# Kernel tuning notes

Hardware: AMD Instinct MI355X
Metric: run time of the kernel (lower is better)

## Reference

```python
import jax, jax.numpy as jnp
import numpy as np

N0, N1, N2 = 409600, 40960, 4096   # source / mid / target node counts per sampled layer
E1, E2 = 409600, 40960             # edges in layer 1 / layer 2
F_IN, F_HID, F_OUT = 512, 256, 128


def setup_inputs() -> dict:
    key = jax.random.key(0)
    ks = jax.random.split(key, 12)
    s = 1.0 / np.sqrt(F_IN)
    s2 = 1.0 / np.sqrt(F_HID)
    return {
        "x": jax.random.normal(ks[0], (N0, F_IN), dtype=jnp.float32),
        "ei1_src": jax.random.randint(ks[1], (E1,), 0, N0),
        "ei1_dst": jax.random.randint(ks[2], (E1,), 0, N1),
        "ei2_src": jax.random.randint(ks[3], (E2,), 0, N1),
        "ei2_dst": jax.random.randint(ks[4], (E2,), 0, N2),
        "W1l": jax.random.uniform(ks[5], (F_IN, F_HID), jnp.float32, -s, s),
        "b1": jax.random.uniform(ks[6], (F_HID,), jnp.float32, -s, s),
        "W1r": jax.random.uniform(ks[7], (F_IN, F_HID), jnp.float32, -s, s),
        "W2l": jax.random.uniform(ks[8], (F_HID, F_OUT), jnp.float32, -s2, s2),
        "b2": jax.random.uniform(ks[9], (F_OUT,), jnp.float32, -s2, s2),
        "W2r": jax.random.uniform(ks[10], (F_HID, F_OUT), jnp.float32, -s2, s2),
    }


def _sage(x_src, src, dst, n_dst, Wl, b, Wr):
    # PyG SAGEConv (mean aggr): out = lin_l(mean_j x_j) + lin_r(x_target)
    msg = x_src[src]                                           # [E, F] gather
    agg = jax.ops.segment_sum(msg, dst, num_segments=n_dst)    # [n_dst, F]
    cnt = jax.ops.segment_sum(jnp.ones((src.shape[0],), x_src.dtype), dst,
                              num_segments=n_dst)
    mean = agg / jnp.maximum(cnt, 1.0)[:, None]
    x_dst = x_src[:n_dst]                                      # targets are first
    return mean @ Wl + b + x_dst @ Wr


def reference(x, ei1_src, ei1_dst, ei2_src, ei2_dst, W1l, b1, W1r, W2l, b2, W2r):
    h = _sage(x, ei1_src, ei1_dst, N1, W1l, b1, W1r)           # [N1, F_HID]
    h = jax.nn.relu(h)                                         # dropout = identity (eval)
    out = _sage(h, ei2_src, ei2_dst, N2, W2l, b2, W2r)         # [N2, F_OUT]
    return out
```

## Files before the change

### kernel.cpp

```cpp
#include <hip/hip_runtime.h>
#include <hip/hip_bf16.h>

#define N0 409600
#define N1 40960
#define N2 4096
#define E1c 409600
#define E2c 40960
#define F_IN 512
#define F_HID 256
#define F_OUT 128

using bf16x8 = __attribute__((ext_vector_type(8))) short;
using f32x4  = __attribute__((ext_vector_type(4))) float;

__device__ __forceinline__ ushort f2bf(float f) {
    union { float f; unsigned u; } v; v.f = f;
    unsigned r = v.u + 0x7fffu + ((v.u >> 16) & 1u);
    return (ushort)(r >> 16);
}
__device__ __forceinline__ float bf2f(ushort b) {
    union { unsigned u; float f; } v; v.u = ((unsigned)b) << 16;
    return v.f;
}

__device__ __forceinline__ bf16x8 load8(const ushort* p) {
    return *(const bf16x8*)p;
}
__device__ __forceinline__ bf16x8 load8(const float* p) {
    float4 a = *(const float4*)p;
    float4 b = *(const float4*)(p + 4);
    bf16x8 r;
    r[0] = (short)f2bf(a.x); r[1] = (short)f2bf(a.y);
    r[2] = (short)f2bf(a.z); r[3] = (short)f2bf(a.w);
    r[4] = (short)f2bf(b.x); r[5] = (short)f2bf(b.y);
    r[6] = (short)f2bf(b.z); r[7] = (short)f2bf(b.w);
    return r;
}

__global__ void k_prep(const int* __restrict__ dst1, int* __restrict__ cnt1,
                       const int* __restrict__ dst2, int* __restrict__ cnt2,
                       const float* __restrict__ W1l, const float* __restrict__ W1r,
                       const float* __restrict__ W2l, const float* __restrict__ W2r,
                       ushort* __restrict__ W1lT, ushort* __restrict__ W1rT,
                       ushort* __restrict__ W2lT, ushort* __restrict__ W2rT) {
    int idx = blockIdx.x * blockDim.x + threadIdx.x;
    if (idx < E1c) atomicAdd(&cnt1[dst1[idx]], 1);
    else if (idx - E1c < E2c) atomicAdd(&cnt2[dst2[idx - E1c]], 1);
    const int S1 = F_IN * F_HID;
    const int S2 = F_HID * F_OUT;
    if (idx < S1) {
        int k = idx / F_HID, n = idx % F_HID;
        W1lT[(size_t)n * F_IN + k] = f2bf(W1l[idx]);
    } else if (idx < 2 * S1) {
        int j = idx - S1;
        int k = j / F_HID, n = j % F_HID;
        W1rT[(size_t)n * F_IN + k] = f2bf(W1r[j]);
    } else if (idx < 2 * S1 + S2) {
        int j = idx - 2 * S1;
        int k = j / F_OUT, n = j % F_OUT;
        W2lT[(size_t)n * F_HID + k] = f2bf(W2l[j]);
    } else if (idx < 2 * S1 + 2 * S2) {
        int j = idx - 2 * S1 - S2;
        int k = j / F_OUT, n = j % F_OUT;
        W2rT[(size_t)n * F_HID + k] = f2bf(W2r[j]);
    }
}

#define NBLK1 (N1 / 1024)
#define NBLK2 (N2 / 1024)

__global__ __launch_bounds__(1024) void k_scanA2(const int* __restrict__ cnt1, int* __restrict__ off1,
                                                 int* __restrict__ bsum1,
                                                 const int* __restrict__ cnt2, int* __restrict__ off2,
                                                 int* __restrict__ bsum2) {
    __shared__ int wsum[16];
    int blk = blockIdx.x;
    const int* cnt; int* off; int* bsum; int lb;
    if (blk < NBLK1) { cnt = cnt1; off = off1; bsum = bsum1; lb = blk; }
    else             { cnt = cnt2; off = off2; bsum = bsum2; lb = blk - NBLK1; }
    int t = threadIdx.x, lane = t & 63, w = t >> 6;
    int i = lb * 1024 + t;
    int v = cnt[i];
    int s = v;
#pragma unroll
    for (int d = 1; d < 64; d <<= 1) {
        int u = __shfl_up(s, d, 64);
        if (lane >= d) s += u;
    }
    if (lane == 63) wsum[w] = s;
    __syncthreads();
    int wpre = 0, total = 0;
#pragma unroll
    for (int j = 0; j < 16; j++) {
        int u = wsum[j];
        if (j < w) wpre += u;
        total += u;
    }
    off[i] = wpre + (s - v);
    if (t == 0) bsum[lb] = total;
}

__global__ __launch_bounds__(1024) void k_scanB2(int* __restrict__ off1, int* __restrict__ cur1,
                                                 const int* __restrict__ bsum1,
                                                 int* __restrict__ off2, int* __restrict__ cur2,
                                                 const int* __restrict__ bsum2) {
    __shared__ int s_pre, s_tot;
    int blk = blockIdx.x;
    int* off; int* cur; const int* bsum; int lb, nblk, n;
    if (blk < NBLK1) { off = off1; cur = cur1; bsum = bsum1; lb = blk;         nblk = NBLK1; n = N1; }
    else             { off = off2; cur = cur2; bsum = bsum2; lb = blk - NBLK1; nblk = NBLK2; n = N2; }
    int t = threadIdx.x;
    if (t < 64) {
        int v = (t < nblk) ? bsum[t] : 0;
        int p = (t < lb) ? v : 0;
        int tt = v;
#pragma unroll
        for (int d = 32; d >= 1; d >>= 1) {
            p  += __shfl_xor(p, d, 64);
            tt += __shfl_xor(tt, d, 64);
        }
        if (t == 0) { s_pre = p; s_tot = tt; }
    }
    __syncthreads();
    int i = lb * 1024 + t;
    int val = off[i] + s_pre;
    off[i] = val;
    cur[i] = val;
    if (lb == 0 && t == 0) off[n] = s_tot;
}

__global__ void k_scatter2(const int* __restrict__ src1, const int* __restrict__ dst1,
                           int* __restrict__ cur1, int* __restrict__ perm1,
                           const int* __restrict__ src2, const int* __restrict__ dst2,
                           int* __restrict__ cur2, int* __restrict__ perm2) {
    int e = blockIdx.x * blockDim.x + threadIdx.x;
    if (e < E1c) {
        int d = dst1[e];
        int pos = atomicAdd(&cur1[d], 1);
        perm1[pos] = src1[e];
    } else {
        int e2 = e - E1c;
        if (e2 < E2c) {
            int d = dst2[e2];
            int pos = atomicAdd(&cur2[d], 1);
            perm2[pos] = src2[e2];
        }
    }
}

__global__ void k_agg1(const float* __restrict__ x, const int* __restrict__ perm,
                       const int* __restrict__ off, ushort* __restrict__ mean) {
    int d = blockIdx.x;
    int beg = off[d], end = off[d + 1];
    int t = threadIdx.x;
    const float4* xp = (const float4*)x;
    float ax = 0.f, ay = 0.f, az = 0.f, aw = 0.f;
    int e = beg;
    for (; e + 3 < end; e += 4) {
        int s0 = perm[e], s1 = perm[e + 1], s2 = perm[e + 2], s3 = perm[e + 3];
        float4 v0 = xp[(size_t)s0 * (F_IN / 4) + t];
        float4 v1 = xp[(size_t)s1 * (F_IN / 4) + t];
        float4 v2 = xp[(size_t)s2 * (F_IN / 4) + t];
        float4 v3 = xp[(size_t)s3 * (F_IN / 4) + t];
        ax += (v0.x + v1.x) + (v2.x + v3.x);
        ay += (v0.y + v1.y) + (v2.y + v3.y);
        az += (v0.z + v1.z) + (v2.z + v3.z);
        aw += (v0.w + v1.w) + (v2.w + v3.w);
    }
    for (; e < end; e++) {
        float4 v0 = xp[(size_t)perm[e] * (F_IN / 4) + t];
        ax += v0.x; ay += v0.y; az += v0.z; aw += v0.w;
    }
    int deg = end - beg;
    float inv = 1.0f / (float)(deg > 0 ? deg : 1);
    ushort4 o;
    o.x = f2bf(ax * inv); o.y = f2bf(ay * inv);
    o.z = f2bf(az * inv); o.w = f2bf(aw * inv);
    ((ushort4*)mean)[(size_t)d * (F_IN / 4) + t] = o;
}

__global__ void k_agg2(const ushort* __restrict__ h, const int* __restrict__ perm,
                       const int* __restrict__ off, ushort* __restrict__ mean) {
    int d = blockIdx.x;
    int beg = off[d], end = off[d + 1];
    int t = threadIdx.x;
    const ushort4* hp = (const ushort4*)h;
    float a0 = 0.f, a1 = 0.f, a2 = 0.f, a3 = 0.f;
    int e = beg;
    for (; e + 3 < end; e += 4) {
        ushort4 v = hp[(size_t)perm[e] * (F_HID / 4) + t];
        ushort4 u = hp[(size_t)perm[e + 1] * (F_HID / 4) + t];
        ushort4 w = hp[(size_t)perm[e + 2] * (F_HID / 4) + t];
        ushort4 z = hp[(size_t)perm[e + 3] * (F_HID / 4) + t];
        a0 += (bf2f(v.x) + bf2f(u.x)) + (bf2f(w.x) + bf2f(z.x));
        a1 += (bf2f(v.y) + bf2f(u.y)) + (bf2f(w.y) + bf2f(z.y));
        a2 += (bf2f(v.z) + bf2f(u.z)) + (bf2f(w.z) + bf2f(z.z));
        a3 += (bf2f(v.w) + bf2f(u.w)) + (bf2f(w.w) + bf2f(z.w));
    }
    for (; e < end; e++) {
        ushort4 v = hp[(size_t)perm[e] * (F_HID / 4) + t];
        a0 += bf2f(v.x); a1 += bf2f(v.y); a2 += bf2f(v.z); a3 += bf2f(v.w);
    }
    int deg = end - beg;
    float inv = 1.0f / (float)(deg > 0 ? deg : 1);
    ushort4 o;
    o.x = f2bf(a0 * inv); o.y = f2bf(a1 * inv);
    o.z = f2bf(a2 * inv); o.w = f2bf(a3 * inv);
    ((ushort4*)mean)[(size_t)d * (F_HID / 4) + t] = o;
}

#define GBK 32
#define APAD 8
template<int WM, int WN, int MF, int NF, int K, int MINW, typename TA2>
__global__ __launch_bounds__(256, MINW) void k_gemm(
    const ushort* __restrict__ A1, const TA2* __restrict__ A2,
    const ushort* __restrict__ B1T, const ushort* __restrict__ B2T,
    const float* __restrict__ bias, int M, int N, int relu,
    ushort* __restrict__ Cb, float* __restrict__ Cf)
{
    constexpr int BM = WM * MF * 16;
    constexpr int BN = WN * NF * 16;
    constexpr int KS = K / GBK;
    constexpr int NS = 2 * KS;
    static_assert(BM % 64 == 0 && BN % 64 == 0, "tile must be multiple of 64");
    __shared__ ushort As[2][BM][GBK + APAD];
    __shared__ ushort Bs[2][BN][GBK + APAD];
    int tid = threadIdx.x;
    int lane = tid & 63;
    int wid = tid >> 6;
    int wm = wid / WN, wn = wid % WN;
    int bm = blockIdx.x * BM, bn = blockIdx.y * BN;

    f32x4 acc[MF][NF];
#pragma unroll
    for (int i = 0; i < MF; i++)
#pragma unroll
        for (int j = 0; j < NF; j++) acc[i][j] = (f32x4){0.f, 0.f, 0.f, 0.f};

    int sr = tid >> 2;
    int sc = (tid & 3) * 8;
    int r0 = lane & 15, kq = (lane >> 4) * 8;

    bf16x8 ra[BM / 64], rb[BN / 64];
#pragma unroll
    for (int i = 0; i < BM / 64; i++)
        ra[i] = load8(A1 + (size_t)(bm + sr + i * 64) * K + sc);
#pragma unroll
    for (int i = 0; i < BN / 64; i++)
        rb[i] = load8(B1T + (size_t)(bn + sr + i * 64) * K + sc);

    for (int s = 0; s < NS; ++s) {
        int buf = s & 1;
#pragma unroll
        for (int i = 0; i < BM / 64; i++) *(bf16x8*)&As[buf][sr + i * 64][sc] = ra[i];
#pragma unroll
        for (int i = 0; i < BN / 64; i++) *(bf16x8*)&Bs[buf][sr + i * 64][sc] = rb[i];
        __syncthreads();
        if (s + 1 < NS) {
            int s1 = s + 1;
            int part1 = (s1 >= KS) ? 1 : 0;
            int k01 = (s1 - part1 * KS) * GBK;
#pragma unroll
            for (int i = 0; i < BM / 64; i++) {
                size_t idx = (size_t)(bm + sr + i * 64) * K + k01 + sc;
                ra[i] = part1 ? load8(A2 + idx) : load8(A1 + idx);
            }
            const ushort* __restrict__ B = part1 ? B2T : B1T;
#pragma unroll
            for (int i = 0; i < BN / 64; i++)
                rb[i] = load8(B + (size_t)(bn + sr + i * 64) * K + k01 + sc);
        }
        bf16x8 af[MF], bfr[NF];
#pragma unroll
        for (int i = 0; i < MF; i++)
            af[i] = *(const bf16x8*)&As[buf][wm * (MF * 16) + i * 16 + r0][kq];
#pragma unroll
        for (int j = 0; j < NF; j++)
            bfr[j] = *(const bf16x8*)&Bs[buf][wn * (NF * 16) + j * 16 + r0][kq];
#pragma unroll
        for (int i = 0; i < MF; i++)
#pragma unroll
            for (int j = 0; j < NF; j++)
                acc[i][j] = __builtin_amdgcn_mfma_f32_16x16x32_bf16(af[i], bfr[j], acc[i][j], 0, 0, 0);
    }

    int cn0 = lane & 15;
    int rq = (lane >> 4) * 4;
#pragma unroll
    for (int i = 0; i < MF; i++) {
#pragma unroll
        for (int j = 0; j < NF; j++) {
            int col = bn + wn * (NF * 16) + j * 16 + cn0;
            float bv = bias[col];
#pragma unroll
            for (int rr = 0; rr < 4; rr++) {
                int row = bm + wm * (MF * 16) + i * 16 + rq + rr;
                float v = acc[i][j][rr] + bv;
                if (relu) v = fmaxf(v, 0.f);
                if (Cb) Cb[(size_t)row * N + col] = f2bf(v);
                if (Cf) Cf[(size_t)row * N + col] = v;
            }
        }
    }
}

static inline size_t align256(size_t x) { return (x + 255) & ~(size_t)255; }

extern "C" void kernel_launch(void* const* d_in, const int* in_sizes, int n_in,
                              void* d_out, int out_size, void* d_ws, size_t ws_size,
                              hipStream_t stream) {
    const float* x = (const float*)d_in[0];
    const int* ei1_src = (const int*)d_in[1];
    const int* ei1_dst = (const int*)d_in[2];
    const int* ei2_src = (const int*)d_in[3];
    const int* ei2_dst = (const int*)d_in[4];
    const float* W1l = (const float*)d_in[5];
    const float* b1 = (const float*)d_in[6];
    const float* W1r = (const float*)d_in[7];
    const float* W2l = (const float*)d_in[8];
    const float* b2 = (const float*)d_in[9];
    const float* W2r = (const float*)d_in[10];
    float* out = (float*)d_out;

    char* p = (char*)d_ws;
    size_t o = 0;
    int* cnt1 = (int*)(p + o); o += (size_t)N1 * 4;
    int* cnt2 = (int*)(p + o); o = align256(o + (size_t)N2 * 4);
    int* off1 = (int*)(p + o); o = align256(o + (size_t)(N1 + 1) * 4);
    int* cur1 = (int*)(p + o); o = align256(o + (size_t)N1 * 4);
    int* perm1 = (int*)(p + o); o = align256(o + (size_t)E1c * 4);
    int* off2 = (int*)(p + o); o = align256(o + (size_t)(N2 + 1) * 4);
    int* cur2 = (int*)(p + o); o = align256(o + (size_t)N2 * 4);
    int* perm2 = (int*)(p + o); o = align256(o + (size_t)E2c * 4);
    int* bsum1 = (int*)(p + o); o = align256(o + 64 * 4);
    int* bsum2 = (int*)(p + o); o = align256(o + 64 * 4);
    ushort* mean1 = (ushort*)(p + o); o = align256(o + (size_t)N1 * F_IN * 2);
    ushort* h     = (ushort*)(p + o); o = align256(o + (size_t)N1 * F_HID * 2);
    ushort* mean2 = (ushort*)(p + o); o = align256(o + (size_t)N2 * F_HID * 2);
    ushort* W1lT  = (ushort*)(p + o); o = align256(o + (size_t)F_IN * F_HID * 2);
    ushort* W1rT  = (ushort*)(p + o); o = align256(o + (size_t)F_IN * F_HID * 2);
    ushort* W2lT  = (ushort*)(p + o); o = align256(o + (size_t)F_HID * F_OUT * 2);
    ushort* W2rT  = (ushort*)(p + o); o = align256(o + (size_t)F_HID * F_OUT * 2);

    hipMemsetAsync(cnt1, 0, (size_t)(N1 + N2) * 4, stream);

    {
        int total = E1c + E2c;
        k_prep<<<(total + 255) / 256, 256, 0, stream>>>(
            ei1_dst, cnt1, ei2_dst, cnt2,
            W1l, W1r, W2l, W2r, W1lT, W1rT, W2lT, W2rT);
    }
    k_scanA2<<<NBLK1 + NBLK2, 1024, 0, stream>>>(cnt1, off1, bsum1, cnt2, off2, bsum2);
    k_scanB2<<<NBLK1 + NBLK2, 1024, 0, stream>>>(off1, cur1, bsum1, off2, cur2, bsum2);
    k_scatter2<<<(E1c + E2c + 255) / 256, 256, 0, stream>>>(
        ei1_src, ei1_dst, cur1, perm1, ei2_src, ei2_dst, cur2, perm2);

    k_agg1<<<N1, F_IN / 4, 0, stream>>>(x, perm1, off1, mean1);
    {
        dim3 grid(N1 / 64, F_HID / 256);
        k_gemm<1, 4, 4, 4, F_IN, 3, float><<<grid, 256, 0, stream>>>(
            mean1, x, W1lT, W1rT, b1, N1, F_HID, 1, h, nullptr);
    }

    k_agg2<<<N2, F_HID / 4, 0, stream>>>(h, perm2, off2, mean2);
    {
        dim3 grid(N2 / 64, F_OUT / 64);
        k_gemm<2, 2, 2, 2, F_HID, 4, ushort><<<grid, 256, 0, stream>>>(
            mean2, h, W2lT, W2rT, b2, N2, F_OUT, 0, nullptr, out);
    }
}
```

Measured before the change: 264.6 us.

## Load GEMM B fragments directly from global to registers and unroll agg1 gather by 8

The GEMM no longer stages the weight (B) tile in shared memory. Each wave loads its MFMA B fragments straight from global memory into registers and double-buffers them across k-steps, which removes the LDS writes and reads for B and frees shared memory. The trade-off is that B data is no longer shared between waves, so global and L2 traffic for weights goes up along with register pressure. The layer-1 aggregation loop is also unrolled to 8 outstanding gathers to expose more memory-level parallelism.

Measured after the change: 278.9 us. 1.05x slower.

```diff
diff --git a/kernel.cpp b/kernel.cpp
--- a/kernel.cpp
+++ b/kernel.cpp
@@ -156,12 +156,25 @@
     const float4* xp = (const float4*)x;
     float ax = 0.f, ay = 0.f, az = 0.f, aw = 0.f;
     int e = beg;
+    for (; e + 7 < end; e += 8) {
+        float4 v0 = xp[(size_t)perm[e]     * (F_IN / 4) + t];
+        float4 v1 = xp[(size_t)perm[e + 1] * (F_IN / 4) + t];
+        float4 v2 = xp[(size_t)perm[e + 2] * (F_IN / 4) + t];
+        float4 v3 = xp[(size_t)perm[e + 3] * (F_IN / 4) + t];
+        float4 v4 = xp[(size_t)perm[e + 4] * (F_IN / 4) + t];
+        float4 v5 = xp[(size_t)perm[e + 5] * (F_IN / 4) + t];
+        float4 v6 = xp[(size_t)perm[e + 6] * (F_IN / 4) + t];
+        float4 v7 = xp[(size_t)perm[e + 7] * (F_IN / 4) + t];
+        ax += ((v0.x + v1.x) + (v2.x + v3.x)) + ((v4.x + v5.x) + (v6.x + v7.x));
+        ay += ((v0.y + v1.y) + (v2.y + v3.y)) + ((v4.y + v5.y) + (v6.y + v7.y));
+        az += ((v0.z + v1.z) + (v2.z + v3.z)) + ((v4.z + v5.z) + (v6.z + v7.z));
+        aw += ((v0.w + v1.w) + (v2.w + v3.w)) + ((v4.w + v5.w) + (v6.w + v7.w));
+    }
     for (; e + 3 < end; e += 4) {
-        int s0 = perm[e], s1 = perm[e + 1], s2 = perm[e + 2], s3 = perm[e + 3];
-        float4 v0 = xp[(size_t)s0 * (F_IN / 4) + t];
-        float4 v1 = xp[(size_t)s1 * (F_IN / 4) + t];
-        float4 v2 = xp[(size_t)s2 * (F_IN / 4) + t];
-        float4 v3 = xp[(size_t)s3 * (F_IN / 4) + t];
+        float4 v0 = xp[(size_t)perm[e]     * (F_IN / 4) + t];
+        float4 v1 = xp[(size_t)perm[e + 1] * (F_IN / 4) + t];
+        float4 v2 = xp[(size_t)perm[e + 2] * (F_IN / 4) + t];
+        float4 v3 = xp[(size_t)perm[e + 3] * (F_IN / 4) + t];
         ax += (v0.x + v1.x) + (v2.x + v3.x);
         ay += (v0.y + v1.y) + (v2.y + v3.y);
         az += (v0.z + v1.z) + (v2.z + v3.z);
@@ -224,7 +237,6 @@
     constexpr int NS = 2 * KS;
     static_assert(BM % 64 == 0 && BN % 64 == 0, "tile must be multiple of 64");
     __shared__ ushort As[2][BM][GBK + APAD];
-    __shared__ ushort Bs[2][BN][GBK + APAD];
     int tid = threadIdx.x;
     int lane = tid & 63;
     int wid = tid >> 6;
@@ -241,20 +253,21 @@
     int sc = (tid & 3) * 8;
     int r0 = lane & 15, kq = (lane >> 4) * 8;
 
-    bf16x8 ra[BM / 64], rb[BN / 64];
+    bf16x8 ra[BM / 64];
+    bf16x8 rbc[NF];
+    bf16x8 rbn[NF];
 #pragma unroll
     for (int i = 0; i < BM / 64; i++)
         ra[i] = load8(A1 + (size_t)(bm + sr + i * 64) * K + sc);
 #pragma unroll
-    for (int i = 0; i < BN / 64; i++)
-        rb[i] = load8(B1T + (size_t)(bn + sr + i * 64) * K + sc);
-
+    for (int j = 0; j < NF; j++)
+        rbc[j] = load8(B1T + (size_t)(bn + wn * (NF * 16) + j * 16 + r0) * K + kq);
+
+#pragma unroll 2
     for (int s = 0; s < NS; ++s) {
         int buf = s & 1;
 #pragma unroll
         for (int i = 0; i < BM / 64; i++) *(bf16x8*)&As[buf][sr + i * 64][sc] = ra[i];
-#pragma unroll
-        for (int i = 0; i < BN / 64; i++) *(bf16x8*)&Bs[buf][sr + i * 64][sc] = rb[i];
         __syncthreads();
         if (s + 1 < NS) {
             int s1 = s + 1;
@@ -267,21 +280,20 @@
             }
             const ushort* __restrict__ B = part1 ? B2T : B1T;
 #pragma unroll
-            for (int i = 0; i < BN / 64; i++)
-                rb[i] = load8(B + (size_t)(bn + sr + i * 64) * K + k01 + sc);
+            for (int j = 0; j < NF; j++)
+                rbn[j] = load8(B + (size_t)(bn + wn * (NF * 16) + j * 16 + r0) * K + k01 + kq);
         }
-        bf16x8 af[MF], bfr[NF];
+        bf16x8 af[MF];
 #pragma unroll
         for (int i = 0; i < MF; i++)
             af[i] = *(const bf16x8*)&As[buf][wm * (MF * 16) + i * 16 + r0][kq];
 #pragma unroll
-        for (int j = 0; j < NF; j++)
-            bfr[j] = *(const bf16x8*)&Bs[buf][wn * (NF * 16) + j * 16 + r0][kq];
-#pragma unroll
         for (int i = 0; i < MF; i++)
 #pragma unroll
             for (int j = 0; j < NF; j++)
-                acc[i][j] = __builtin_amdgcn_mfma_f32_16x16x32_bf16(af[i], bfr[j], acc[i][j], 0, 0, 0);
+                acc[i][j] = __builtin_amdgcn_mfma_f32_16x16x32_bf16(af[i], rbc[j], acc[i][j], 0, 0, 0);
+#pragma unroll
+        for (int j = 0; j < NF; j++) rbc[j] = rbn[j];
     }
 
     int cn0 = lane & 15;
```
